# Optimization experiments

Hardware: AMD Instinct MI355X
Metric: run time of the kernel (lower is better)

## Reference

```python
import jax, jax.numpy as jnp
import numpy as np

B, N, F_IN, F_OUT = 64, 1024, 256, 64


def setup_inputs() -> dict:
    key = jax.random.key(0)
    k1, k2, k3, k4 = jax.random.split(key, 4)
    # xavier_uniform with gain=1.414 ~= sqrt(2): limit = gain*sqrt(6/(fan_in+fan_out))
    limW = 1.414 * np.sqrt(6.0 / (F_IN + F_OUT))
    lima = 1.414 * np.sqrt(6.0 / (2 * F_OUT + 1))
    return {
        "input": jax.random.normal(k1, (B, N, F_IN), dtype=jnp.float32),
        "adj": jax.random.randint(k2, (B, N, N), 0, 2, dtype=jnp.int32),
        "W": jax.random.uniform(k3, (F_IN, F_OUT), jnp.float32, -limW, limW),
        "a": jax.random.uniform(k4, (2 * F_OUT, 1), jnp.float32, -lima, lima),
    }


def reference(input, adj, W, a):
    # h = input @ W : (B, N, Fo)
    h = jnp.matmul(input, W)
    Bs, n, Fo = h.shape
    a1 = a[:Fo, 0]   # applied to the (scrambled) left block of a_input
    a2 = a[Fo:, 0]   # applied to the tiled right block

    # The original builds a_input by repeat_interleave(N, dim=2).view -> the left
    # block's row (i*N + j) holds h[b, i, (j*Fo + t)//N] for t in [0, Fo).
    # Its dot with a1 is therefore h[b, i, :] @ M[j, :] with
    #   M[j, f] = sum_{t : (j*Fo+t)//N == f} a1[t]
    idx = (jnp.arange(n)[:, None] * Fo + jnp.arange(Fo)[None, :]) // n  # (N, Fo), values in [0, Fo)
    rows = jnp.broadcast_to(jnp.arange(n)[:, None], (n, Fo))
    M = jnp.zeros((n, Fo), h.dtype).at[rows, idx].add(jnp.broadcast_to(a1, (n, Fo)))  # (N, Fo)

    e1 = jnp.einsum("bif,jf->bij", h, M)          # left-block contribution, (B, N, N)
    e2 = jnp.einsum("bjf,f->bj", h, a2)           # right block = h tiled over i, (B, N)
    # leakyrelu result is immediately overwritten by relu in the source; only relu matters
    e = jax.nn.relu(e1 + e2[:, None, :])

    neg = jnp.asarray(-9e15, e.dtype)
    attention = jax.nn.softmax(jnp.where(adj > 0, e, neg), axis=2)
    # F.dropout omitted (inference / deterministic reference)
    h_prime = jnp.matmul(attention, h)            # (B, N, Fo)
    return jax.nn.elu(h_prime)                    # concat=True branch
```

## Files before the change

### kernel.cpp

```cpp
#include <hip/hip_runtime.h>
#include <math.h>

#define B_   64
#define N_   1024
#define FIN_ 256
#define FO_  64

typedef __attribute__((ext_vector_type(4))) float f32x4;
typedef __attribute__((ext_vector_type(8))) short short8;

__device__ __forceinline__ unsigned short f2bf_rne(float f) {
    union { float f; unsigned u; } v; v.f = f;
    const unsigned r = v.u + 0x7fffu + ((v.u >> 16) & 1u);
    return (unsigned short)(r >> 16);
}
__device__ __forceinline__ float bf2f(unsigned short h) {
    union { unsigned u; float f; } v; v.u = ((unsigned)h) << 16;
    return v.f;
}

__global__ void k0_wt(const float* __restrict__ W,
                      unsigned short* __restrict__ WThi,
                      unsigned short* __restrict__ WTlo)
{
    const int idx = blockIdx.x * 256 + threadIdx.x;
    const int k = idx >> 6, f = idx & 63;
    const float w = W[idx];
    const unsigned short hi = f2bf_rne(w);
    const unsigned short lo = f2bf_rne(w - bf2f(hi));
    WThi[f * FIN_ + k] = hi;
    WTlo[f * FIN_ + k] = lo;
}

__global__ __launch_bounds__(256, 4) void k1_hproj(
    const float* __restrict__ input,
    const unsigned short* __restrict__ WThi,
    const unsigned short* __restrict__ WTlo,
    const float* __restrict__ a,
    unsigned short* __restrict__ hbT,
    unsigned short* __restrict__ hrT,
    float* __restrict__ e2)
{
    __shared__ union {
        struct { unsigned short Ahi[64*64], Alo[64*64], Bhi[64*64], Blo[64*64]; } s;
        struct { unsigned short hb[64*72], hr[64*72]; } e;
    } u;

    const int t  = threadIdx.x;
    const int r0 = blockIdx.x * 64;
    const int b  = blockIdx.x >> 4;
    const int jb = r0 & (N_ - 1);

    const int l = t & 63, lm = l & 15, lk = l >> 4, wm0 = (t >> 6) * 16;

    f32x4 acc[4] = {};
    float4 iv[2][2];
    short8 wh[2], wl[2];

    auto load_chunk = [&](int c0) {
        #pragma unroll
        for (int q = 0; q < 2; ++q) {
            const int ci = t * 2 + q;
            const int row = ci >> 3, cc = ci & 7;
            iv[q][0] = *reinterpret_cast<const float4*>(
                &input[(size_t)(r0 + row) * FIN_ + c0 + cc * 8]);
            iv[q][1] = *reinterpret_cast<const float4*>(
                &input[(size_t)(r0 + row) * FIN_ + c0 + cc * 8 + 4]);
            wh[q] = *reinterpret_cast<const short8*>(&WThi[row * FIN_ + c0 + cc * 8]);
            wl[q] = *reinterpret_cast<const short8*>(&WTlo[row * FIN_ + c0 + cc * 8]);
        }
    };
    auto store_chunk = [&]() {
        #pragma unroll
        for (int q = 0; q < 2; ++q) {
            const int ci = t * 2 + q;
            const int row = ci >> 3, cc = ci & 7;
            const int pos = (cc ^ (row & 7)) * 8;
            alignas(16) float xv[8];
            *reinterpret_cast<float4*>(&xv[0]) = iv[q][0];
            *reinterpret_cast<float4*>(&xv[4]) = iv[q][1];
            alignas(16) unsigned short h8[8], l8[8];
            #pragma unroll
            for (int e = 0; e < 8; ++e) {
                h8[e] = f2bf_rne(xv[e]);
                l8[e] = f2bf_rne(xv[e] - bf2f(h8[e]));
            }
            *reinterpret_cast<short8*>(&u.s.Ahi[row * 64 + pos]) = *reinterpret_cast<short8*>(h8);
            *reinterpret_cast<short8*>(&u.s.Alo[row * 64 + pos]) = *reinterpret_cast<short8*>(l8);
            *reinterpret_cast<short8*>(&u.s.Bhi[row * 64 + pos]) = wh[q];
            *reinterpret_cast<short8*>(&u.s.Blo[row * 64 + pos]) = wl[q];
        }
    };
    auto compute = [&]() {
        #pragma unroll
        for (int ks = 0; ks < 2; ++ks) {
            const int mrow = wm0 + lm;
            const int ac = (((ks << 2) + lk) ^ (mrow & 7)) * 8;
            const short8 ah = *reinterpret_cast<const short8*>(&u.s.Ahi[mrow * 64 + ac]);
            const short8 al = *reinterpret_cast<const short8*>(&u.s.Alo[mrow * 64 + ac]);
            #pragma unroll
            for (int nt = 0; nt < 4; ++nt) {
                const int fr = nt * 16 + lm;
                const int bc = (((ks << 2) + lk) ^ (fr & 7)) * 8;
                const short8 bh = *reinterpret_cast<const short8*>(&u.s.Bhi[fr * 64 + bc]);
                const short8 bl = *reinterpret_cast<const short8*>(&u.s.Blo[fr * 64 + bc]);
                acc[nt] = __builtin_amdgcn_mfma_f32_16x16x32_bf16(ah, bh, acc[nt], 0, 0, 0);
                acc[nt] = __builtin_amdgcn_mfma_f32_16x16x32_bf16(ah, bl, acc[nt], 0, 0, 0);
                acc[nt] = __builtin_amdgcn_mfma_f32_16x16x32_bf16(al, bh, acc[nt], 0, 0, 0);
            }
        }
    };

    load_chunk(0);
    #pragma unroll 1
    for (int c = 0; c < 4; ++c) {
        store_chunk();
        __syncthreads();
        if (c < 3) load_chunk((c + 1) * 64);
        compute();
        __syncthreads();
    }

    float ap[4];
    #pragma unroll
    for (int nt = 0; nt < 4; ++nt) ap[nt] = a[FO_ + nt * 16 + lm];

    #pragma unroll
    for (int reg = 0; reg < 4; ++reg) {
        const int row = wm0 + lk * 4 + reg;
        float e2p = 0.f;
        #pragma unroll
        for (int nt = 0; nt < 4; ++nt) {
            const float hv = acc[nt][reg];
            e2p += hv * ap[nt];
            const unsigned short hh = f2bf_rne(hv);
            const unsigned short hr = f2bf_rne(hv - bf2f(hh));
            const int f = nt * 16 + lm;
            u.e.hb[f * 72 + row] = hh;
            u.e.hr[f * 72 + row] = hr;
        }
        e2p += __shfl_xor(e2p, 1);
        e2p += __shfl_xor(e2p, 2);
        e2p += __shfl_xor(e2p, 4);
        e2p += __shfl_xor(e2p, 8);
        if (lm == 0) e2[r0 + row] = e2p;
    }
    __syncthreads();

    {
        const int f = t >> 2, seg = t & 3;
        const size_t gb = ((size_t)(b * FO_ + f)) * N_ + jb + seg * 16;
        *reinterpret_cast<short8*>(&hbT[gb]) =
            *reinterpret_cast<const short8*>(&u.e.hb[f * 72 + seg * 16]);
        *reinterpret_cast<short8*>(&hbT[gb + 8]) =
            *reinterpret_cast<const short8*>(&u.e.hb[f * 72 + seg * 16 + 8]);
        *reinterpret_cast<short8*>(&hrT[gb]) =
            *reinterpret_cast<const short8*>(&u.e.hr[f * 72 + seg * 16]);
        *reinterpret_cast<short8*>(&hrT[gb + 8]) =
            *reinterpret_cast<const short8*>(&u.e.hr[f * 72 + seg * 16 + 8]);
    }
}

__global__ __launch_bounds__(256, 4) void k2_attn(
    const unsigned short* __restrict__ hbT,
    const unsigned short* __restrict__ hrT,
    const int*   __restrict__ adj,
    const float* __restrict__ a,
    const float* __restrict__ e2,
    float* __restrict__ out)
{
    __shared__ unsigned short whi_lds[2][64*32], wlo_lds[2][64*32];
    __shared__ unsigned short hb_lds [2][64*32], hr_lds [2][64*32];
    __shared__ float den_lds[64][4];

    const int t  = threadIdx.x;
    const int b  = blockIdx.y;
    const int i0 = blockIdx.x * 64;

    const int wi = t >> 2, ws = t & 3, jl0 = ws * 8;
    const int l = t & 63, lm = l & 15, lk = l >> 4, wm0 = (t >> 6) * 16;

    const int*   adjrow = adj + ((size_t)b * N_ + i0 + wi) * N_;
    const float* e2b    = e2 + (size_t)b * N_;
    const unsigned short* hbTb = hbT + (size_t)b * FO_ * N_;
    const unsigned short* hrTb = hrT + (size_t)b * FO_ * N_;

    float S1 = 0.f;
    #pragma unroll
    for (int f = 0; f < FO_; f += 4) {
        const float4 av = *reinterpret_cast<const float4*>(&a[f]);
        S1 += av.x + av.y + av.z + av.w;
    }

    f32x4 acc[4] = {};
    float denreg = 0.f;

    int4   areg[2];
    short8 hbreg, hrreg;
    float4 e2r[2];
    float  c2r;

    auto prefetch = [&](int tile) {
        const int jt = tile * 32;
        areg[0] = *reinterpret_cast<const int4*>(&adjrow[jt + jl0]);
        areg[1] = *reinterpret_cast<const int4*>(&adjrow[jt + jl0 + 4]);
        hbreg = *reinterpret_cast<const short8*>(&hbTb[(size_t)wi * N_ + jt + ws * 8]);
        hrreg = *reinterpret_cast<const short8*>(&hrTb[(size_t)wi * N_ + jt + ws * 8]);
        e2r[0] = *reinterpret_cast<const float4*>(&e2b[jt + jl0]);
        e2r[1] = *reinterpret_cast<const float4*>(&e2b[jt + jl0 + 4]);
        const int g = (jt >> 4) + (ws >> 1);
        c2r = bf2f(hbTb[(size_t)g * N_ + i0 + wi]) + bf2f(hrTb[(size_t)g * N_ + i0 + wi]);
    };

    auto phaseW = [&](int buf) {
        *reinterpret_cast<short8*>(&hb_lds[buf][wi * 32 + ws * 8]) = hbreg;
        *reinterpret_cast<short8*>(&hr_lds[buf][wi * 32 + ws * 8]) = hrreg;
        const float cg = S1 * c2r;
        const int aa[8] = { areg[0].x, areg[0].y, areg[0].z, areg[0].w,
                            areg[1].x, areg[1].y, areg[1].z, areg[1].w };
        alignas(16) float ee[8];
        *reinterpret_cast<float4*>(&ee[0]) = e2r[0];
        *reinterpret_cast<float4*>(&ee[4]) = e2r[1];
        alignas(16) unsigned short w_hi[8], w_lo[8];
        #pragma unroll
        for (int d = 0; d < 8; ++d) {
            const float ev = fmaxf(cg + ee[d], 0.f);
            const float w  = aa[d] ? __expf(ev) : 0.f;
            const unsigned short hi = f2bf_rne(w);
            const unsigned short lo = f2bf_rne(w - bf2f(hi));
            w_hi[d] = hi; w_lo[d] = lo;
            denreg += bf2f(hi) + bf2f(lo);
        }
        *reinterpret_cast<short8*>(&whi_lds[buf][wi * 32 + jl0]) = *reinterpret_cast<short8*>(w_hi);
        *reinterpret_cast<short8*>(&wlo_lds[buf][wi * 32 + jl0]) = *reinterpret_cast<short8*>(w_lo);
    };

    auto phaseG = [&](int buf) {
        const short8 awh = *reinterpret_cast<const short8*>(&whi_lds[buf][(wm0 + lm) * 32 + lk * 8]);
        const short8 awl = *reinterpret_cast<const short8*>(&wlo_lds[buf][(wm0 + lm) * 32 + lk * 8]);
        #pragma unroll
        for (int nt = 0; nt < 4; ++nt) {
            const int fr = nt * 16 + lm;
            const short8 bh = *reinterpret_cast<const short8*>(&hb_lds[buf][fr * 32 + lk * 8]);
            const short8 br = *reinterpret_cast<const short8*>(&hr_lds[buf][fr * 32 + lk * 8]);
            acc[nt] = __builtin_amdgcn_mfma_f32_16x16x32_bf16(awh, bh, acc[nt], 0, 0, 0);
            acc[nt] = __builtin_amdgcn_mfma_f32_16x16x32_bf16(awh, br, acc[nt], 0, 0, 0);
            acc[nt] = __builtin_amdgcn_mfma_f32_16x16x32_bf16(awl, bh, acc[nt], 0, 0, 0);
        }
    };

    prefetch(0);
    phaseW(0);
    prefetch(1);
    __syncthreads();

    int cur = 0;
    #pragma unroll 1
    for (int tile = 0; tile < 32; ++tile) {
        if (tile < 31) phaseW(cur ^ 1);
        if (tile < 30) prefetch(tile + 2);
        phaseG(cur);
        __syncthreads();
        cur ^= 1;
    }

    den_lds[wi][ws] = denreg;
    __syncthreads();

    #pragma unroll
    for (int reg = 0; reg < 4; ++reg) {
        const int i = wm0 + lk * 4 + reg;
        const float4 dv = *reinterpret_cast<const float4*>(&den_lds[i][0]);
        const float inv = 1.0f / (dv.x + dv.y + dv.z + dv.w);
        #pragma unroll
        for (int nt = 0; nt < 4; ++nt) {
            const float x = acc[nt][reg] * inv;
            const float y = (x > 0.f) ? x : expm1f(x);
            out[((size_t)b * N_ + i0 + i) * FO_ + nt * 16 + lm] = y;
        }
    }
}

extern "C" void kernel_launch(void* const* d_in, const int* in_sizes, int n_in,
                              void* d_out, int out_size, void* d_ws, size_t ws_size,
                              hipStream_t stream) {
    const float* input = (const float*)d_in[0];
    const int*   adj   = (const int*)d_in[1];
    const float* W     = (const float*)d_in[2];
    const float* a     = (const float*)d_in[3];
    float* out = (float*)d_out;

    char* ws = (char*)d_ws;
    unsigned short* hbT  = (unsigned short*)(ws);
    unsigned short* hrT  = (unsigned short*)(ws + (8u << 20));
    float*          e2   = (float*)(ws + (16u << 20));
    unsigned short* WThi = (unsigned short*)(ws + (16u << 20) + (256u << 10));
    unsigned short* WTlo = WThi + FO_ * FIN_;

    k0_wt  <<<dim3(64),                 dim3(256), 0, stream>>>(W, WThi, WTlo);
    k1_hproj<<<dim3((B_ * N_) / 64),    dim3(256), 0, stream>>>(input, WThi, WTlo, a, hbT, hrT, e2);
    k2_attn<<<dim3(N_ / 64, B_),        dim3(256), 0, stream>>>(hbT, hrT, adj, a, e2, out);
}
```

Baseline: 442.2 us.

## Drop LDS staging; load MFMA operands directly from global and truncate bf16 splits

Both the projection and attention kernels now build MFMA operand fragments directly in registers from global memory, with no LDS double-buffering or block barriers. The attention kernel computes softmax weights per MFMA lane layout and reduces the denominator with shuffles instead of an LDS array. Round-to-nearest bf16 hi/lo splitting is replaced by bit truncation, which cuts ALU work but changes rounding slightly. The cost is redundant global and L2 traffic: each wave refetches the hbT/hrT and W tiles that were previously shared through LDS, and the loads are no longer coalesced in the same way.

```diff
diff --git a/kernel.cpp b/kernel.cpp
--- a/kernel.cpp
+++ b/kernel.cpp
@@ -9,15 +9,15 @@
 typedef __attribute__((ext_vector_type(4))) float f32x4;
 typedef __attribute__((ext_vector_type(8))) short short8;
 
-__device__ __forceinline__ unsigned short f2bf_rne(float f) {
-    union { float f; unsigned u; } v; v.f = f;
-    const unsigned r = v.u + 0x7fffu + ((v.u >> 16) & 1u);
-    return (unsigned short)(r >> 16);
-}
-__device__ __forceinline__ float bf2f(unsigned short h) {
-    union { unsigned u; float f; } v; v.u = ((unsigned)h) << 16;
-    return v.f;
-}
+__device__ __forceinline__ unsigned fbits(float f){ union{float f;unsigned u;}v; v.f=f; return v.u; }
+__device__ __forceinline__ float bcast(unsigned u){ union{unsigned u;float f;}v; v.u=u; return v.f; }
+__device__ __forceinline__ float bf2f(unsigned short h){ return bcast(((unsigned)h)<<16); }
+__device__ __forceinline__ float hi_part(float x){ return bcast(fbits(x) & 0xffff0000u); }
+__device__ __forceinline__ unsigned pack_hi(float x0, float x1){
+    return (fbits(x1) & 0xffff0000u) | (fbits(x0) >> 16);
+}
+
+union U8 { unsigned u[4]; short8 s8; };
 
 __global__ void k0_wt(const float* __restrict__ W,
                       unsigned short* __restrict__ WThi,
@@ -26,10 +26,9 @@
     const int idx = blockIdx.x * 256 + threadIdx.x;
     const int k = idx >> 6, f = idx & 63;
     const float w = W[idx];
-    const unsigned short hi = f2bf_rne(w);
-    const unsigned short lo = f2bf_rne(w - bf2f(hi));
-    WThi[f * FIN_ + k] = hi;
-    WTlo[f * FIN_ + k] = lo;
+    const float hf = hi_part(w);
+    WThi[f * FIN_ + k] = (unsigned short)(fbits(w) >> 16);
+    WTlo[f * FIN_ + k] = (unsigned short)(fbits(w - hf) >> 16);
 }
 
 __global__ __launch_bounds__(256, 4) void k1_hproj(
@@ -41,84 +40,44 @@
     unsigned short* __restrict__ hrT,
     float* __restrict__ e2)
 {
-    __shared__ union {
-        struct { unsigned short Ahi[64*64], Alo[64*64], Bhi[64*64], Blo[64*64]; } s;
-        struct { unsigned short hb[64*72], hr[64*72]; } e;
-    } u;
+    __shared__ unsigned short eb[64 * 72];
+    __shared__ unsigned short er[64 * 72];
 
     const int t  = threadIdx.x;
+    const int lm = t & 15, lk = (t >> 4) & 3, wm0 = (t >> 6) * 16;
     const int r0 = blockIdx.x * 64;
     const int b  = blockIdx.x >> 4;
     const int jb = r0 & (N_ - 1);
 
-    const int l = t & 63, lm = l & 15, lk = l >> 4, wm0 = (t >> 6) * 16;
+    const float* arow = input + (size_t)(r0 + wm0 + lm) * FIN_;
 
     f32x4 acc[4] = {};
-    float4 iv[2][2];
-    short8 wh[2], wl[2];
-
-    auto load_chunk = [&](int c0) {
-        #pragma unroll
-        for (int q = 0; q < 2; ++q) {
-            const int ci = t * 2 + q;
-            const int row = ci >> 3, cc = ci & 7;
-            iv[q][0] = *reinterpret_cast<const float4*>(
-                &input[(size_t)(r0 + row) * FIN_ + c0 + cc * 8]);
-            iv[q][1] = *reinterpret_cast<const float4*>(
-                &input[(size_t)(r0 + row) * FIN_ + c0 + cc * 8 + 4]);
-            wh[q] = *reinterpret_cast<const short8*>(&WThi[row * FIN_ + c0 + cc * 8]);
-            wl[q] = *reinterpret_cast<const short8*>(&WTlo[row * FIN_ + c0 + cc * 8]);
-        }
-    };
-    auto store_chunk = [&]() {
-        #pragma unroll
-        for (int q = 0; q < 2; ++q) {
-            const int ci = t * 2 + q;
-            const int row = ci >> 3, cc = ci & 7;
-            const int pos = (cc ^ (row & 7)) * 8;
-            alignas(16) float xv[8];
-            *reinterpret_cast<float4*>(&xv[0]) = iv[q][0];
-            *reinterpret_cast<float4*>(&xv[4]) = iv[q][1];
-            alignas(16) unsigned short h8[8], l8[8];
-            #pragma unroll
-            for (int e = 0; e < 8; ++e) {
-                h8[e] = f2bf_rne(xv[e]);
-                l8[e] = f2bf_rne(xv[e] - bf2f(h8[e]));
-            }
-            *reinterpret_cast<short8*>(&u.s.Ahi[row * 64 + pos]) = *reinterpret_cast<short8*>(h8);
-            *reinterpret_cast<short8*>(&u.s.Alo[row * 64 + pos]) = *reinterpret_cast<short8*>(l8);
-            *reinterpret_cast<short8*>(&u.s.Bhi[row * 64 + pos]) = wh[q];
-            *reinterpret_cast<short8*>(&u.s.Blo[row * 64 + pos]) = wl[q];
-        }
-    };
-    auto compute = [&]() {
-        #pragma unroll
-        for (int ks = 0; ks < 2; ++ks) {
-            const int mrow = wm0 + lm;
-            const int ac = (((ks << 2) + lk) ^ (mrow & 7)) * 8;
-            const short8 ah = *reinterpret_cast<const short8*>(&u.s.Ahi[mrow * 64 + ac]);
-            const short8 al = *reinterpret_cast<const short8*>(&u.s.Alo[mrow * 64 + ac]);
-            #pragma unroll
-            for (int nt = 0; nt < 4; ++nt) {
-                const int fr = nt * 16 + lm;
-                const int bc = (((ks << 2) + lk) ^ (fr & 7)) * 8;
-                const short8 bh = *reinterpret_cast<const short8*>(&u.s.Bhi[fr * 64 + bc]);
-                const short8 bl = *reinterpret_cast<const short8*>(&u.s.Blo[fr * 64 + bc]);
-                acc[nt] = __builtin_amdgcn_mfma_f32_16x16x32_bf16(ah, bh, acc[nt], 0, 0, 0);
-                acc[nt] = __builtin_amdgcn_mfma_f32_16x16x32_bf16(ah, bl, acc[nt], 0, 0, 0);
-                acc[nt] = __builtin_amdgcn_mfma_f32_16x16x32_bf16(al, bh, acc[nt], 0, 0, 0);
-            }
-        }
-    };
-
-    load_chunk(0);
-    #pragma unroll 1
-    for (int c = 0; c < 4; ++c) {
-        store_chunk();
-        __syncthreads();
-        if (c < 3) load_chunk((c + 1) * 64);
-        compute();
-        __syncthreads();
+    float4 xa = *reinterpret_cast<const float4*>(&arow[lk * 8]);
+    float4 xb = *reinterpret_cast<const float4*>(&arow[lk * 8 + 4]);
+
+    #pragma unroll
+    for (int ks = 0; ks < 8; ++ks) {
+        const float x[8] = { xa.x, xa.y, xa.z, xa.w, xb.x, xb.y, xb.z, xb.w };
+        U8 ah, al;
+        #pragma unroll
+        for (int p = 0; p < 4; ++p) {
+            const float f0 = x[2 * p], f1 = x[2 * p + 1];
+            ah.u[p] = pack_hi(f0, f1);
+            al.u[p] = pack_hi(f0 - hi_part(f0), f1 - hi_part(f1));
+        }
+        if (ks < 7) {
+            xa = *reinterpret_cast<const float4*>(&arow[(ks + 1) * 32 + lk * 8]);
+            xb = *reinterpret_cast<const float4*>(&arow[(ks + 1) * 32 + lk * 8 + 4]);
+        }
+        #pragma unroll
+        for (int nt = 0; nt < 4; ++nt) {
+            const int off = (nt * 16 + lm) * FIN_ + ks * 32 + lk * 8;
+            const short8 bh = *reinterpret_cast<const short8*>(&WThi[off]);
+            const short8 bl = *reinterpret_cast<const short8*>(&WTlo[off]);
+            acc[nt] = __builtin_amdgcn_mfma_f32_16x16x32_bf16(ah.s8, bh, acc[nt], 0, 0, 0);
+            acc[nt] = __builtin_amdgcn_mfma_f32_16x16x32_bf16(ah.s8, bl, acc[nt], 0, 0, 0);
+            acc[nt] = __builtin_amdgcn_mfma_f32_16x16x32_bf16(al.s8, bh, acc[nt], 0, 0, 0);
+        }
     }
 
     float ap[4];
@@ -133,11 +92,10 @@
         for (int nt = 0; nt < 4; ++nt) {
             const float hv = acc[nt][reg];
             e2p += hv * ap[nt];
-            const unsigned short hh = f2bf_rne(hv);
-            const unsigned short hr = f2bf_rne(hv - bf2f(hh));
+            const float hf = hi_part(hv);
             const int f = nt * 16 + lm;
-            u.e.hb[f * 72 + row] = hh;
-            u.e.hr[f * 72 + row] = hr;
+            eb[f * 72 + row] = (unsigned short)(fbits(hv) >> 16);
+            er[f * 72 + row] = (unsigned short)(fbits(hv - hf) >> 16);
         }
         e2p += __shfl_xor(e2p, 1);
         e2p += __shfl_xor(e2p, 2);
@@ -151,13 +109,13 @@
         const int f = t >> 2, seg = t & 3;
         const size_t gb = ((size_t)(b * FO_ + f)) * N_ + jb + seg * 16;
         *reinterpret_cast<short8*>(&hbT[gb]) =
-            *reinterpret_cast<const short8*>(&u.e.hb[f * 72 + seg * 16]);
+            *reinterpret_cast<const short8*>(&eb[f * 72 + seg * 16]);
         *reinterpret_cast<short8*>(&hbT[gb + 8]) =
-            *reinterpret_cast<const short8*>(&u.e.hb[f * 72 + seg * 16 + 8]);
+            *reinterpret_cast<const short8*>(&eb[f * 72 + seg * 16 + 8]);
         *reinterpret_cast<short8*>(&hrT[gb]) =
-            *reinterpret_cast<const short8*>(&u.e.hr[f * 72 + seg * 16]);
+            *reinterpret_cast<const short8*>(&er[f * 72 + seg * 16]);
         *reinterpret_cast<short8*>(&hrT[gb + 8]) =
-            *reinterpret_cast<const short8*>(&u.e.hr[f * 72 + seg * 16 + 8]);
+            *reinterpret_cast<const short8*>(&er[f * 72 + seg * 16 + 8]);
     }
 }
 
@@ -169,18 +127,13 @@
     const float* __restrict__ e2,
     float* __restrict__ out)
 {
-    __shared__ unsigned short whi_lds[2][64*32], wlo_lds[2][64*32];
-    __shared__ unsigned short hb_lds [2][64*32], hr_lds [2][64*32];
-    __shared__ float den_lds[64][4];
-
     const int t  = threadIdx.x;
+    const int lm = t & 15, lk = (t >> 4) & 3, wm0 = (t >> 6) * 16;
     const int b  = blockIdx.y;
     const int i0 = blockIdx.x * 64;
-
-    const int wi = t >> 2, ws = t & 3, jl0 = ws * 8;
-    const int l = t & 63, lm = l & 15, lk = l >> 4, wm0 = (t >> 6) * 16;
-
-    const int*   adjrow = adj + ((size_t)b * N_ + i0 + wi) * N_;
+    const int irow = i0 + wm0 + lm;
+
+    const int*   adjrow = adj + ((size_t)b * N_ + irow) * N_;
     const float* e2b    = e2 + (size_t)b * N_;
     const unsigned short* hbTb = hbT + (size_t)b * FO_ * N_;
     const unsigned short* hrTb = hrT + (size_t)b * FO_ * N_;
@@ -193,90 +146,69 @@
     }
 
     f32x4 acc[4] = {};
-    float denreg = 0.f;
-
-    int4   areg[2];
-    short8 hbreg, hrreg;
-    float4 e2r[2];
-    float  c2r;
-
-    auto prefetch = [&](int tile) {
+    float den = 0.f;
+
+    int4 aC0 = *reinterpret_cast<const int4*>(&adjrow[lk * 8]);
+    int4 aC1 = *reinterpret_cast<const int4*>(&adjrow[lk * 8 + 4]);
+
+    #pragma unroll 1
+    for (int tile = 0; tile < 32; ++tile) {
         const int jt = tile * 32;
-        areg[0] = *reinterpret_cast<const int4*>(&adjrow[jt + jl0]);
-        areg[1] = *reinterpret_cast<const int4*>(&adjrow[jt + jl0 + 4]);
-        hbreg = *reinterpret_cast<const short8*>(&hbTb[(size_t)wi * N_ + jt + ws * 8]);
-        hrreg = *reinterpret_cast<const short8*>(&hrTb[(size_t)wi * N_ + jt + ws * 8]);
-        e2r[0] = *reinterpret_cast<const float4*>(&e2b[jt + jl0]);
-        e2r[1] = *reinterpret_cast<const float4*>(&e2b[jt + jl0 + 4]);
-        const int g = (jt >> 4) + (ws >> 1);
-        c2r = bf2f(hbTb[(size_t)g * N_ + i0 + wi]) + bf2f(hrTb[(size_t)g * N_ + i0 + wi]);
-    };
-
-    auto phaseW = [&](int buf) {
-        *reinterpret_cast<short8*>(&hb_lds[buf][wi * 32 + ws * 8]) = hbreg;
-        *reinterpret_cast<short8*>(&hr_lds[buf][wi * 32 + ws * 8]) = hrreg;
-        const float cg = S1 * c2r;
-        const int aa[8] = { areg[0].x, areg[0].y, areg[0].z, areg[0].w,
-                            areg[1].x, areg[1].y, areg[1].z, areg[1].w };
-        alignas(16) float ee[8];
-        *reinterpret_cast<float4*>(&ee[0]) = e2r[0];
-        *reinterpret_cast<float4*>(&ee[4]) = e2r[1];
-        alignas(16) unsigned short w_hi[8], w_lo[8];
+        int4 aN0, aN1;
+        if (tile < 31) {
+            aN0 = *reinterpret_cast<const int4*>(&adjrow[jt + 32 + lk * 8]);
+            aN1 = *reinterpret_cast<const int4*>(&adjrow[jt + 32 + lk * 8 + 4]);
+        }
+        const float4 ea = *reinterpret_cast<const float4*>(&e2b[jt + lk * 8]);
+        const float4 eb2 = *reinterpret_cast<const float4*>(&e2b[jt + lk * 8 + 4]);
+        const int g = (jt >> 4) + (lk >> 1);
+        const float c2 = bf2f(hbTb[(size_t)g * N_ + irow]) +
+                         bf2f(hrTb[(size_t)g * N_ + irow]);
+        const float cg = S1 * c2;
+
+        const int   aa[8] = { aC0.x, aC0.y, aC0.z, aC0.w, aC1.x, aC1.y, aC1.z, aC1.w };
+        const float ee[8] = { ea.x, ea.y, ea.z, ea.w, eb2.x, eb2.y, eb2.z, eb2.w };
+        float hf[8], lf[8];
         #pragma unroll
         for (int d = 0; d < 8; ++d) {
             const float ev = fmaxf(cg + ee[d], 0.f);
             const float w  = aa[d] ? __expf(ev) : 0.f;
-            const unsigned short hi = f2bf_rne(w);
-            const unsigned short lo = f2bf_rne(w - bf2f(hi));
-            w_hi[d] = hi; w_lo[d] = lo;
-            denreg += bf2f(hi) + bf2f(lo);
-        }
-        *reinterpret_cast<short8*>(&whi_lds[buf][wi * 32 + jl0]) = *reinterpret_cast<short8*>(w_hi);
-        *reinterpret_cast<short8*>(&wlo_lds[buf][wi * 32 + jl0]) = *reinterpret_cast<short8*>(w_lo);
-    };
-
-    auto phaseG = [&](int buf) {
-        const short8 awh = *reinterpret_cast<const short8*>(&whi_lds[buf][(wm0 + lm) * 32 + lk * 8]);
-        const short8 awl = *reinterpret_cast<const short8*>(&wlo_lds[buf][(wm0 + lm) * 32 + lk * 8]);
-        #pragma unroll
-        for (int nt = 0; nt < 4; ++nt) {
-            const int fr = nt * 16 + lm;
-            const short8 bh = *reinterpret_cast<const short8*>(&hb_lds[buf][fr * 32 + lk * 8]);
-            const short8 br = *reinterpret_cast<const short8*>(&hr_lds[buf][fr * 32 + lk * 8]);
-            acc[nt] = __builtin_amdgcn_mfma_f32_16x16x32_bf16(awh, bh, acc[nt], 0, 0, 0);
-            acc[nt] = __builtin_amdgcn_mfma_f32_16x16x32_bf16(awh, br, acc[nt], 0, 0, 0);
-            acc[nt] = __builtin_amdgcn_mfma_f32_16x16x32_bf16(awl, bh, acc[nt], 0, 0, 0);
-        }
-    };
-
-    prefetch(0);
-    phaseW(0);
-    prefetch(1);
-    __syncthreads();
-
-    int cur = 0;
-    #pragma unroll 1
-    for (int tile = 0; tile < 32; ++tile) {
-        if (tile < 31) phaseW(cur ^ 1);
-        if (tile < 30) prefetch(tile + 2);
-        phaseG(cur);
-        __syncthreads();
-        cur ^= 1;
-    }
-
-    den_lds[wi][ws] = denreg;
-    __syncthreads();
+            hf[d] = hi_part(w);
+            lf[d] = w - hf[d];
+            den += hf[d] + hi_part(lf[d]);
+        }
+        U8 whi, wlo;
+        #pragma unroll
+        for (int p = 0; p < 4; ++p) {
+            whi.u[p] = pack_hi(hf[2 * p], hf[2 * p + 1]);
+            wlo.u[p] = pack_hi(lf[2 * p], lf[2 * p + 1]);
+        }
+
+        #pragma unroll
+        for (int nt = 0; nt < 4; ++nt) {
+            const size_t off = (size_t)(nt * 16 + lm) * N_ + jt + lk * 8;
+            const short8 bh = *reinterpret_cast<const short8*>(&hbTb[off]);
+            const short8 br = *reinterpret_cast<const short8*>(&hrTb[off]);
+            acc[nt] = __builtin_amdgcn_mfma_f32_16x16x32_bf16(whi.s8, bh, acc[nt], 0, 0, 0);
+            acc[nt] = __builtin_amdgcn_mfma_f32_16x16x32_bf16(whi.s8, br, acc[nt], 0, 0, 0);
+            acc[nt] = __builtin_amdgcn_mfma_f32_16x16x32_bf16(wlo.s8, bh, acc[nt], 0, 0, 0);
+        }
+        aC0 = aN0; aC1 = aN1;
+    }
+
+    den += __shfl_xor(den, 16);
+    den += __shfl_xor(den, 32);
 
     #pragma unroll
     for (int reg = 0; reg < 4; ++reg) {
-        const int i = wm0 + lk * 4 + reg;
-        const float4 dv = *reinterpret_cast<const float4*>(&den_lds[i][0]);
-        const float inv = 1.0f / (dv.x + dv.y + dv.z + dv.w);
+        const int m = lk * 4 + reg;
+        const float dm = __shfl(den, m);
+        const float inv = 1.0f / dm;
         #pragma unroll
         for (int nt = 0; nt < 4; ++nt) {
             const float x = acc[nt][reg] * inv;
             const float y = (x > 0.f) ? x : expm1f(x);
-            out[((size_t)b * N_ + i0 + i) * FO_ + nt * 16 + lm] = y;
+            out[((size_t)b * N_ + i0 + wm0 + m) * FO_ + nt * 16 + lm] = y;
         }
     }
 }
@@ -297,7 +229,7 @@
     unsigned short* WThi = (unsigned short*)(ws + (16u << 20) + (256u << 10));
     unsigned short* WTlo = WThi + FO_ * FIN_;
 
-    k0_wt  <<<dim3(64),                 dim3(256), 0, stream>>>(W, WThi, WTlo);
-    k1_hproj<<<dim3((B_ * N_) / 64),    dim3(256), 0, stream>>>(input, WThi, WTlo, a, hbT, hrT, e2);
-    k2_attn<<<dim3(N_ / 64, B_),        dim3(256), 0, stream>>>(hbT, hrT, adj, a, e2, out);
-}
+    k0_wt   <<<dim3(64),              dim3(256), 0, stream>>>(W, WThi, WTlo);
+    k1_hproj<<<dim3((B_ * N_) / 64),  dim3(256), 0, stream>>>(input, WThi, WTlo, a, hbT, hrT, e2);
+    k2_attn <<<dim3(N_ / 64, B_),     dim3(256), 0, stream>>>(hbT, hrT, adj, a, e2, out);
+}
```

New measurement: 533.6 us. 1.21x slower.
